# Kernel tuning notes

Hardware: AMD Instinct MI355X
Metric: run time of the kernel (lower is better)

The kernel has to match this reference:

```python
import jax, jax.numpy as jnp
import numpy as np

# MoE config (matches init_kwargs)
E = 32      # num_experts
K = 4       # num_experts_per_tok (top_k)
H = 1024    # hidden_size
I = 512     # moe_intermediate_size (shared expert uses I * num_shared_experts = I)
B, S = 2, 2048
T = B * S
C = 1024
ROUTED_SCALE = 1.0


def _silu_and_mul(gu):
    g, u = jnp.split(gu, 2, axis=-1)
    return jax.nn.silu(g) * u


def setup_inputs() -> dict:
    key = jax.random.key(0)
    ks = jax.random.split(key, 6)
    s = 0.02
    return {
        "hidden_states": jax.random.normal(ks[0], (B, S, H), jnp.float32),
        "gate_w": jax.random.normal(ks[1], (E, H), jnp.float32) * s,
        "w_gate_up": jax.random.normal(ks[2], (E, H, 2 * I), jnp.float32) * s,
        "w_down": jax.random.normal(ks[3], (E, I, H), jnp.float32) * s,
        "shared_w_gate_up": jax.random.normal(ks[4], (H, 2 * I), jnp.float32) * s,
        "shared_w_down": jax.random.normal(ks[5], (I, H), jnp.float32) * s,
    }


def reference(hidden_states, gate_w, w_gate_up, w_down, shared_w_gate_up, shared_w_down):
    b, s, h = hidden_states.shape
    x = hidden_states.reshape(-1, h)                      # [T, H]
    t = x.shape[0]

    # --- router: gate linear -> softmax -> top-k -> renormalize ---
    logits = x @ gate_w.T                                 # [T, E]
    probs = jax.nn.softmax(logits, axis=-1)
    topk_w, topk_idx = jax.lax.top_k(probs, K)            # [T, K]
    topk_w = topk_w / jnp.sum(topk_w, axis=-1, keepdims=True)  # norm_topk_prob
    topk_w = topk_w * ROUTED_SCALE

    # --- dispatch: sort (token, slot) assignments by expert, scatter into capacity buffer ---
    e_flat = topk_idx.reshape(-1)                         # [T*K]
    w_flat = topk_w.reshape(-1)
    t_flat = jnp.repeat(jnp.arange(t), K)
    order = jnp.argsort(e_flat)                           # stable sort by expert id
    e_s, w_s, t_s = e_flat[order], w_flat[order], t_flat[order]
    counts = jax.ops.segment_sum(jnp.ones_like(e_s), e_s, num_segments=E)
    starts = jnp.cumsum(counts) - counts                  # exclusive prefix sum
    pos = jnp.arange(t * K) - starts[e_s]                 # position within expert group
    slot = jnp.minimum(pos, C)                            # overflow -> trash slot C
    buf = jnp.zeros((E, C + 1, h), x.dtype).at[e_s, slot].set(x[t_s])

    # --- grouped expert MLP (silu-gated) ---
    gu = jnp.einsum('ech,ehi->eci', buf[:, :C], w_gate_up)        # [E, C, 2I]
    expert_out = jnp.einsum('eci,eih->ech', _silu_and_mul(gu), w_down)  # [E, C, H]
    expert_out = jnp.pad(expert_out, ((0, 0), (0, 1), (0, 0)))    # trash slot reads zero

    # --- combine: gather back, weight, scatter-add per token ---
    gate = jnp.where(pos < C, w_s, 0.0)[:, None]
    routed = jnp.zeros_like(x).at[t_s].add(expert_out[e_s, slot] * gate)

    # --- shared expert MLP ---
    shared = _silu_and_mul(x @ shared_w_gate_up) @ shared_w_down

    return (routed + shared).reshape(b, s, h)
```

## Files before the change

### kernel.cpp

```cpp
#include <hip/hip_runtime.h>
#include <cstdint>
#include <cstddef>

#define NEXP   32
#define TOPK   4
#define HD     1024
#define ID     512
#define TT     4096
#define CAP    1024
#define SHARED_BASE (NEXP*CAP)
#define NSLOT  (NEXP*CAP + TT)
#define MAXTILES 320

#define KSPLIT 16
#define KCH    64
#define KSUB   32

typedef __attribute__((ext_vector_type(4))) float f32x4;
typedef __bf16 bf16x8 __attribute__((ext_vector_type(8)));

__device__ __forceinline__ unsigned short f2bf(float f) {
    union { float f; unsigned int u; } v; v.f = f;
    unsigned int u = v.u;
    u = (u + 0x7FFFu + ((u >> 16) & 1u)) >> 16;
    return (unsigned short)u;
}
__device__ __forceinline__ float bf2f(unsigned short s) {
    union { unsigned int u; float f; } v; v.u = ((unsigned int)s) << 16;
    return v.f;
}

#define GLOAD_LDS16(g, l)                                                     \
    __builtin_amdgcn_global_load_lds(                                         \
        (__attribute__((address_space(1))) void*)(g),                         \
        (__attribute__((address_space(3))) void*)(l), 16, 0, 0)

__global__ void k_transpose_bf16(const float* __restrict__ src,
                                 const float* __restrict__ srcS,
                                 unsigned short* __restrict__ dst,
                                 int K, int N) {
    __shared__ float ld[64][65];
    const size_t esz = (size_t)K * N;
    const int z = blockIdx.z;
    const float* s = (z < NEXP) ? src + (size_t)z * esz : srcS;
    dst += (size_t)z * esz;
    const int n0 = blockIdx.x * 64, k0 = blockIdx.y * 64;
    const int tid = threadIdx.x;
    const int c4 = (tid & 15) * 4;
    const int rbase = tid >> 4;
#pragma unroll
    for (int p = 0; p < 4; p++) {
        int row = rbase + p * 16;
        float4 v = *(const float4*)(s + (size_t)(k0 + row) * N + n0 + c4);
        ld[row][c4 + 0] = v.x; ld[row][c4 + 1] = v.y;
        ld[row][c4 + 2] = v.z; ld[row][c4 + 3] = v.w;
    }
    __syncthreads();
    const int n  = tid >> 2;
    const int ks = (tid & 3) * 16;
    unsigned short tmp[16];
#pragma unroll
    for (int i = 0; i < 16; i++) tmp[i] = f2bf(ld[ks + i][n]);
    uint4 a, b;
    a.x = tmp[0] | (tmp[1] << 16);  a.y = tmp[2] | (tmp[3] << 16);
    a.z = tmp[4] | (tmp[5] << 16);  a.w = tmp[6] | (tmp[7] << 16);
    b.x = tmp[8] | (tmp[9] << 16);  b.y = tmp[10] | (tmp[11] << 16);
    b.z = tmp[12] | (tmp[13] << 16); b.w = tmp[14] | (tmp[15] << 16);
    unsigned short* op = dst + (size_t)(n0 + n) * K + k0 + ks;
    *(uint4*)op = a;
    *(uint4*)(op + 8) = b;
}

__global__ __launch_bounds__(256)
void k_logits(const float* __restrict__ x, const float* __restrict__ gw,
              float* __restrict__ part, unsigned short* __restrict__ xb) {
    __shared__ float xsT[KSUB][260];
    __shared__ float gsT[KSUB][36];
    const int tid = threadIdx.x;
    const int lane = tid & 63, wv = tid >> 6;
    const int tg = lane >> 2, eg = lane & 3;
    const int t0 = blockIdx.x * 256;
    const int kbase = blockIdx.y * KCH;
    const int tbase = wv * 64 + tg * 4;
    const int ebase = eg * 8;

    float acc[4][8];
#pragma unroll
    for (int j = 0; j < 4; j++)
#pragma unroll
        for (int i = 0; i < 8; i++) acc[j][i] = 0.f;

    for (int ks = 0; ks < KCH; ks += KSUB) {
        const int k0 = kbase + ks;
        if (ks > 0) __syncthreads();
#pragma unroll
        for (int p = 0; p < 8; p++) {
            int vid = p * 256 + tid;
            int t = vid >> 3, kq = (vid & 7) * 4;
            float4 v = *(const float4*)(x + (size_t)(t0 + t) * HD + k0 + kq);
            xsT[kq + 0][t] = v.x; xsT[kq + 1][t] = v.y;
            xsT[kq + 2][t] = v.z; xsT[kq + 3][t] = v.w;
            ushort4 o;
            o.x = f2bf(v.x); o.y = f2bf(v.y); o.z = f2bf(v.z); o.w = f2bf(v.w);
            *(ushort4*)(xb + (size_t)(t0 + t) * HD + k0 + kq) = o;
        }
#pragma unroll
        for (int p = 0; p < 4; p++) {
            int vid = p * 256 + tid;
            int e = vid >> 5, k = vid & 31;
            gsT[k][e] = gw[(size_t)e * HD + k0 + k];
        }
        __syncthreads();
#pragma unroll 4
        for (int k = 0; k < KSUB; k++) {
            float4 xv = *(const float4*)&xsT[k][tbase];
            float4 g0 = *(const float4*)&gsT[k][ebase];
            float4 g1 = *(const float4*)&gsT[k][ebase + 4];
            float xa[4] = {xv.x, xv.y, xv.z, xv.w};
#pragma unroll
            for (int j = 0; j < 4; j++) {
                acc[j][0] += xa[j] * g0.x; acc[j][1] += xa[j] * g0.y;
                acc[j][2] += xa[j] * g0.z; acc[j][3] += xa[j] * g0.w;
                acc[j][4] += xa[j] * g1.x; acc[j][5] += xa[j] * g1.y;
                acc[j][6] += xa[j] * g1.z; acc[j][7] += xa[j] * g1.w;
            }
        }
    }
    const size_t base = ((size_t)blockIdx.y * TT + (t0 + tbase)) * 32 + ebase;
#pragma unroll
    for (int j = 0; j < 4; j++) {
        float4 w0, w1;
        w0.x = acc[j][0]; w0.y = acc[j][1]; w0.z = acc[j][2]; w0.w = acc[j][3];
        w1.x = acc[j][4]; w1.y = acc[j][5]; w1.z = acc[j][6]; w1.w = acc[j][7];
        *(float4*)(part + base + (size_t)j * 32) = w0;
        *(float4*)(part + base + (size_t)j * 32 + 4) = w1;
    }
}

__global__ __launch_bounds__(256)
void k_topk(const float* __restrict__ part,
            int* __restrict__ choice, float* __restrict__ cw,
            int* __restrict__ tok, float* __restrict__ wgt) {
    const int lane = threadIdx.x & 63, wv = threadIdx.x >> 6;
    const int t = blockIdx.x * 4 + wv;
    const int e = lane & 31;
    const int sbase = (lane >> 5) * 8;
    float v = 0.f;
#pragma unroll
    for (int s = 0; s < 8; s++)
        v += part[((size_t)(sbase + s) * TT + t) * 32 + e];
    v += __shfl_xor(v, 32);
    float sc = (lane < 32) ? v : -INFINITY;

    float lv[TOPK]; int le[TOPK];
#pragma unroll
    for (int r = 0; r < TOPK; r++) {
        float m = sc;
#pragma unroll
        for (int d = 1; d < 64; d <<= 1) m = fmaxf(m, __shfl_xor(m, d));
        unsigned long long ball = __ballot(sc == m);
        int widx = __ffsll(ball) - 1;
        lv[r] = m; le[r] = widx;
        if (lane == widx) sc = -INFINITY;
    }
    if (lane == 0) {
        float wv4[TOPK], wsum = 0.f;
#pragma unroll
        for (int r = 0; r < TOPK; r++) { wv4[r] = __expf(lv[r] - lv[0]); wsum += wv4[r]; }
#pragma unroll
        for (int r = 0; r < TOPK; r++) {
            choice[t * TOPK + r] = le[r];
            cw[t * TOPK + r] = wv4[r] / wsum;
        }
        tok[SHARED_BASE + t] = t;
        wgt[SHARED_BASE + t] = 1.0f;
    }
}

__global__ __launch_bounds__(1024)
void k_assign(const int* __restrict__ choice, const float* __restrict__ cw,
              int* __restrict__ cnt, int* __restrict__ tok,
              float* __restrict__ wgt, int* __restrict__ smap) {
    const int e = blockIdx.x;
    const int tid = threadIdx.x, lane = tid & 63, wv = tid >> 6;
    __shared__ int wtot[16];
    int running = 0;
    for (int it = 0; it < (TT * TOPK) / 1024; it++) {
        const int i = it * 1024 + tid;
        const bool match = (choice[i] == e);
        unsigned long long ball = __ballot(match);
        int wt = __popcll(ball);
        int wpre = __popcll(ball & ((1ull << lane) - 1ull));
        if (lane == 0) wtot[wv] = wt;
        __syncthreads();
        int woff = 0, tot = 0;
#pragma unroll
        for (int w = 0; w < 16; w++) { int c = wtot[w]; tot += c; if (w < wv) woff += c; }
        int pos = running + woff + wpre;
        running += tot;
        __syncthreads();
        if (match) {
            if (pos < CAP) {
                int slot = e * CAP + pos;
                tok[slot] = i >> 2;
                wgt[slot] = cw[i];
                smap[i] = slot;
            } else {
                smap[i] = -1;
            }
        }
    }
    if (tid == 0) cnt[e] = min(running, CAP);
}

template <int KD, bool GATHER, bool SILU>
__global__ __launch_bounds__(256)
void k_moe_gemm(const unsigned short* __restrict__ Ab,
                const unsigned short* __restrict__ Bt,
                unsigned short* __restrict__ Cout,
                const int* __restrict__ tok,
                const int* __restrict__ cnt) {
    const int tid  = threadIdx.x;
    const int lane = tid & 63;
    const int wv   = tid >> 6;

    int c_l = (lane < NEXP) ? min(cnt[lane], CAP) : ((lane == NEXP) ? TT : 0);
    int nt_l = (c_l + 127) >> 7;
    int pre = nt_l;
#pragma unroll
    for (int d = 1; d < 64; d <<= 1) {
        int up = __shfl_up(pre, d);
        if (lane >= d) pre += up;
    }
    const int ntl = __shfl(pre, 63);
    const int chunk = (ntl + 7) >> 3;
    const int c_xcd = blockIdx.x;
    const int qy = blockIdx.y;
    if ((qy >> 3) >= chunk) return;
    const int j = c_xcd * chunk + (qy >> 3);
    if (j >= ntl) return;
    const int nt = qy & 7;
    const int start_l = pre - nt_l;
    const bool mine = (j >= start_l) && (j < start_l + nt_l);
    const unsigned long long bl = __ballot(mine);
    const int e_lane = __ffsll((long long)bl) - 1;
    const int e  = e_lane;
    const int mt = j - __shfl(start_l, e_lane);
    const int cE = __shfl(c_l, e_lane);

    const int slotbase = (e < NEXP) ? e * CAP : SHARED_BASE;
    const int m0 = mt * 128;
    const int rowsv = min(128, cE - m0);

    const unsigned short* Bte = Bt + (size_t)e * (1024 * KD);

    __shared__ unsigned short As[3][128 * 32];
    __shared__ unsigned short Bs[3][128 * 32];

    const int rr  = lane >> 2;
    const int seg = (lane & 3) ^ ((lane >> 3) & 3);
    const int r0 = wv * 32 + rr;
    const int r1 = r0 + 16;

    int ga0 = m0 + r0, ga1 = m0 + r1;
    int ra0, ra1;
    if (GATHER) {
        ra0 = (ga0 < cE) ? tok[slotbase + ga0] : 0;
        ra1 = (ga1 < cE) ? tok[slotbase + ga1] : 0;
    } else {
        ra0 = slotbase + ga0;
        ra1 = slotbase + ga1;
    }
    const unsigned short* ap0 = Ab + (size_t)ra0 * KD + seg * 8;
    const unsigned short* ap1 = Ab + (size_t)ra1 * KD + seg * 8;

    int br0, br1;
    if (SILU) {
        int in0 = r0 & 63, in1 = r1 & 63;
        int c0 = nt * 64 + (r0 >> 6) * 32 + (in0 & 31);
        int c1 = nt * 64 + (r1 >> 6) * 32 + (in1 & 31);
        br0 = (in0 < 32) ? c0 : 512 + c0;
        br1 = (in1 < 32) ? c1 : 512 + c1;
    } else {
        br0 = nt * 128 + r0;
        br1 = nt * 128 + r1;
    }
    const unsigned short* bp0 = Bte + (size_t)br0 * KD + seg * 8;
    const unsigned short* bp1 = Bte + (size_t)br1 * KD + seg * 8;

    const int aoff0 = (wv * 32) * 32, aoff1 = (wv * 32 + 16) * 32;

    f32x4 acc[4][4];
#pragma unroll
    for (int i = 0; i < 4; i++)
#pragma unroll
        for (int j2 = 0; j2 < 4; j2++) acc[i][j2] = (f32x4)(0.0f);

    const int mrow = lane & 15;
    const int quad = lane >> 4;
    const int wm = wv >> 1, wn = wv & 1;
    const int sw = (quad ^ ((mrow >> 1) & 3)) * 8;

    const int aRdOff = (wm * 64 + mrow) * 32 + sw;
    const int bRdOff = (wn * 64 + mrow) * 32 + sw;

    GLOAD_LDS16(ap0, As[0] + aoff0);
    GLOAD_LDS16(ap1, As[0] + aoff1);
    GLOAD_LDS16(bp0, Bs[0] + aoff0);
    GLOAD_LDS16(bp1, Bs[0] + aoff1);
    GLOAD_LDS16(ap0 + 32, As[1] + aoff0);
    GLOAD_LDS16(ap1 + 32, As[1] + aoff1);
    GLOAD_LDS16(bp0 + 32, Bs[1] + aoff0);
    GLOAD_LDS16(bp1 + 32, Bs[1] + aoff1);

    int p = 0;
    for (int k0 = 0; k0 < KD; k0 += 32) {
        if (k0 + 32 < KD) {
            asm volatile("s_waitcnt vmcnt(4) lgkmcnt(0)" ::: "memory");
        } else {
            asm volatile("s_waitcnt vmcnt(0) lgkmcnt(0)" ::: "memory");
        }
        __builtin_amdgcn_s_barrier();
        asm volatile("" ::: "memory");

        const int kn = k0 + 64;
        if (kn < KD) {
            int pw = p + 2; if (pw >= 3) pw -= 3;
            GLOAD_LDS16(ap0 + kn, As[pw] + aoff0);
            GLOAD_LDS16(ap1 + kn, As[pw] + aoff1);
            GLOAD_LDS16(bp0 + kn, Bs[pw] + aoff0);
            GLOAD_LDS16(bp1 + kn, Bs[pw] + aoff1);
        }

        bf16x8 af[4], bf[4];
#pragma unroll
        for (int i = 0; i < 4; i++) {
            af[i] = *(const bf16x8*)(As[p] + aRdOff + i * 16 * 32);
            bf[i] = *(const bf16x8*)(Bs[p] + bRdOff + i * 16 * 32);
        }
#pragma unroll
        for (int mi = 0; mi < 4; mi++)
#pragma unroll
            for (int nj = 0; nj < 4; nj++)
                acc[mi][nj] = __builtin_amdgcn_mfma_f32_16x16x32_bf16(
                    af[mi], bf[nj], acc[mi][nj], 0, 0, 0);
        p++; if (p >= 3) p = 0;
    }

    if (SILU) {
#pragma unroll
        for (int mi = 0; mi < 4; mi++)
#pragma unroll
            for (int nj = 0; nj < 2; nj++) {
                f32x4 g = acc[mi][nj];
                f32x4 u = acc[mi][nj + 2];
#pragma unroll
                for (int r = 0; r < 4; r++) {
                    int rloc = wm * 64 + mi * 16 + quad * 4 + r;
                    if (rloc < rowsv) {
                        float gv = g[r], uv = u[r];
                        float a = (gv / (1.f + __expf(-gv))) * uv;
                        int c = nt * 64 + wn * 32 + nj * 16 + mrow;
                        Cout[(size_t)(slotbase + m0 + rloc) * ID + c] = f2bf(a);
                    }
                }
            }
    } else {
#pragma unroll
        for (int mi = 0; mi < 4; mi++)
#pragma unroll
            for (int nj = 0; nj < 4; nj++) {
                f32x4 v = acc[mi][nj];
#pragma unroll
                for (int r = 0; r < 4; r++) {
                    int rloc = wm * 64 + mi * 16 + quad * 4 + r;
                    if (rloc < rowsv) {
                        int c = nt * 128 + wn * 64 + nj * 16 + mrow;
                        Cout[(size_t)(slotbase + m0 + rloc) * HD + c] = f2bf(v[r]);
                    }
                }
            }
    }
}

__global__ __launch_bounds__(256)
void k_combine(const unsigned short* __restrict__ eout,
               const int* __restrict__ smap,
               const float* __restrict__ wgt,
               float* __restrict__ out) {
    const int t = blockIdx.x;
    const int h0 = threadIdx.x * 4;
    ushort4 q = *(const ushort4*)(eout + (size_t)(SHARED_BASE + t) * HD + h0);
    float a0 = bf2f(q.x), a1 = bf2f(q.y), a2 = bf2f(q.z), a3 = bf2f(q.w);
#pragma unroll
    for (int r = 0; r < TOPK; r++) {
        int slot = smap[t * TOPK + r];
        if (slot >= 0) {
            float w = wgt[slot];
            ushort4 e4 = *(const ushort4*)(eout + (size_t)slot * HD + h0);
            a0 += w * bf2f(e4.x); a1 += w * bf2f(e4.y);
            a2 += w * bf2f(e4.z); a3 += w * bf2f(e4.w);
        }
    }
    float4 o; o.x = a0; o.y = a1; o.z = a2; o.w = a3;
    *(float4*)(out + (size_t)t * HD + h0) = o;
}

extern "C" void kernel_launch(void* const* d_in, const int* in_sizes, int n_in,
                              void* d_out, int out_size, void* d_ws, size_t ws_size,
                              hipStream_t stream) {
    const float* x   = (const float*)d_in[0];
    const float* gw  = (const float*)d_in[1];
    const float* wgu = (const float*)d_in[2];
    const float* wdn = (const float*)d_in[3];
    const float* sgu = (const float*)d_in[4];
    const float* sdn = (const float*)d_in[5];
    float* out = (float*)d_out;

    char* w = (char*)d_ws;
    size_t off = 0;
    int* cnt = (int*)(w + off);                       off += 256;
    unsigned short* xb     = (unsigned short*)(w + off); off += (size_t)TT * HD * 2;
    unsigned short* wgup_t = (unsigned short*)(w + off); off += (size_t)33 * 1024 * 1024 * 2;
    unsigned short* wdn_t  = (unsigned short*)(w + off); off += (size_t)33 * 1024 * 512 * 2;
    unsigned short* act    = (unsigned short*)(w + off); off += (size_t)NSLOT * ID * 2;
    unsigned short* eout   = (unsigned short*)(w + off); off += (size_t)NSLOT * HD * 2;
    int*   tok    = (int*)(w + off);   off += (size_t)NSLOT * 4;
    float* wgt    = (float*)(w + off); off += (size_t)NSLOT * 4;
    int*   smap   = (int*)(w + off);   off += (size_t)TT * TOPK * 4;
    int*   choice = (int*)(w + off);   off += (size_t)TT * TOPK * 4;
    float* cw     = (float*)(w + off); off += (size_t)TT * TOPK * 4;

    float* part = (float*)eout;

    k_transpose_bf16<<<dim3(16, 16, 33), 256, 0, stream>>>(wgu, sgu, wgup_t, 1024, 1024);
    k_transpose_bf16<<<dim3(16, 8, 33),  256, 0, stream>>>(wdn, sdn, wdn_t, 512, 1024);

    k_logits<<<dim3(16, KSPLIT), 256, 0, stream>>>(x, gw, part, xb);
    k_topk<<<TT / 4, 256, 0, stream>>>(part, choice, cw, tok, wgt);
    k_assign<<<NEXP, 1024, 0, stream>>>(choice, cw, cnt, tok, wgt, smap);

    k_moe_gemm<1024, true, true><<<dim3(8, MAXTILES), 256, 0, stream>>>(xb, wgup_t, act, tok, cnt);
    k_moe_gemm<512, false, false><<<dim3(8, MAXTILES), 256, 0, stream>>>(act, wdn_t, eout, tok, cnt);

    k_combine<<<TT, 256, 0, stream>>>(eout, smap, wgt, out);
}
```

Before: 430.9 us.

## Enlarge MoE GEMM tiles to 256x256 with 8 waves and 4-stage pipeline

The grouped expert GEMMs now use 256x256 output tiles computed by 512-thread blocks (8 waves, each covering 128x64), instead of 128x128 tiles with 4 waves. The K loop becomes a 4-buffer LDS pipeline with split A/B prefetch, interleaved half-tile MFMA phases, s_setprio and explicit barriers. The aim is more data reuse per tile and better overlap of loads with MFMA work. In exchange it uses more LDS (128KB) and registers, allowing only one block per CU, and partial tiles on experts with few tokens waste more work with fewer total tiles.

```diff
diff --git a/kernel.cpp b/kernel.cpp
--- a/kernel.cpp
+++ b/kernel.cpp
@@ -10,7 +10,7 @@
 #define CAP    1024
 #define SHARED_BASE (NEXP*CAP)
 #define NSLOT  (NEXP*CAP + TT)
-#define MAXTILES 320
+#define GRIDY  80
 
 #define KSPLIT 16
 #define KCH    64
@@ -213,8 +213,59 @@
     if (tid == 0) cnt[e] = min(running, CAP);
 }
 
+#define GEMM_ITER(T, PF, W)                                                    \
+{                                                                              \
+    const unsigned short* Ar = &As[(T) & 3][0];                                \
+    const unsigned short* Br = &Bs[(T) & 3][0];                                \
+    const int kn = ((T) + 3) * 32;                                             \
+    bf16x8 af[8], bf[4];                                                       \
+    _Pragma("unroll")                                                          \
+    for (int i = 0; i < 4; i++) {                                              \
+        af[i] = *(const bf16x8*)(Ar + aRdOff + i * 512);                       \
+        bf[i] = *(const bf16x8*)(Br + bRdOff + i * 512);                       \
+    }                                                                          \
+    if (PF) {                                                                  \
+        GLOAD_LDS16(ap0 + kn, &As[((T) + 3) & 3][0] + aoff0);                  \
+        GLOAD_LDS16(ap1 + kn, &As[((T) + 3) & 3][0] + aoff1);                  \
+    }                                                                          \
+    __builtin_amdgcn_s_barrier();                                              \
+    asm volatile("s_waitcnt lgkmcnt(0)" ::: "memory");                         \
+    __builtin_amdgcn_sched_barrier(0);                                         \
+    __builtin_amdgcn_s_setprio(1);                                             \
+    _Pragma("unroll")                                                          \
+    for (int mi = 0; mi < 4; mi++)                                             \
+        _Pragma("unroll")                                                      \
+        for (int nj = 0; nj < 4; nj++)                                         \
+            acc[mi][nj] = __builtin_amdgcn_mfma_f32_16x16x32_bf16(             \
+                af[mi], bf[nj], acc[mi][nj], 0, 0, 0);                         \
+    __builtin_amdgcn_s_setprio(0);                                             \
+    __builtin_amdgcn_s_barrier();                                              \
+    _Pragma("unroll")                                                          \
+    for (int i = 4; i < 8; i++)                                                \
+        af[i] = *(const bf16x8*)(Ar + aRdOff + i * 512);                       \
+    if (PF) {                                                                  \
+        GLOAD_LDS16(bp0 + kn, &Bs[((T) + 3) & 3][0] + aoff0);                  \
+        GLOAD_LDS16(bp1 + kn, &Bs[((T) + 3) & 3][0] + aoff1);                  \
+    }                                                                          \
+    __builtin_amdgcn_s_barrier();                                              \
+    asm volatile("s_waitcnt lgkmcnt(0)" ::: "memory");                         \
+    __builtin_amdgcn_sched_barrier(0);                                         \
+    __builtin_amdgcn_s_setprio(1);                                             \
+    _Pragma("unroll")                                                          \
+    for (int mi = 4; mi < 8; mi++)                                             \
+        _Pragma("unroll")                                                      \
+        for (int nj = 0; nj < 4; nj++)                                         \
+            acc[mi][nj] = __builtin_amdgcn_mfma_f32_16x16x32_bf16(             \
+                af[mi], bf[nj], acc[mi][nj], 0, 0, 0);                         \
+    __builtin_amdgcn_s_setprio(0);                                             \
+    if ((W) == 8)      asm volatile("s_waitcnt vmcnt(8)" ::: "memory");        \
+    else if ((W) == 4) asm volatile("s_waitcnt vmcnt(4)" ::: "memory");        \
+    else if ((W) == 0) asm volatile("s_waitcnt vmcnt(0)" ::: "memory");        \
+    if ((W) >= 0) __builtin_amdgcn_s_barrier();                                \
+}
+
 template <int KD, bool GATHER, bool SILU>
-__global__ __launch_bounds__(256)
+__global__ __launch_bounds__(512, 1)
 void k_moe_gemm(const unsigned short* __restrict__ Ab,
                 const unsigned short* __restrict__ Bt,
                 unsigned short* __restrict__ Cout,
@@ -225,7 +276,7 @@
     const int wv   = tid >> 6;
 
     int c_l = (lane < NEXP) ? min(cnt[lane], CAP) : ((lane == NEXP) ? TT : 0);
-    int nt_l = (c_l + 127) >> 7;
+    int nt_l = (c_l + 255) >> 8;
     int pre = nt_l;
 #pragma unroll
     for (int d = 1; d < 64; d <<= 1) {
@@ -236,10 +287,10 @@
     const int chunk = (ntl + 7) >> 3;
     const int c_xcd = blockIdx.x;
     const int qy = blockIdx.y;
-    if ((qy >> 3) >= chunk) return;
-    const int j = c_xcd * chunk + (qy >> 3);
+    if ((qy >> 2) >= chunk) return;
+    const int j = c_xcd * chunk + (qy >> 2);
     if (j >= ntl) return;
-    const int nt = qy & 7;
+    const int nt = qy & 3;
     const int start_l = pre - nt_l;
     const bool mine = (j >= start_l) && (j < start_l + nt_l);
     const unsigned long long bl = __ballot(mine);
@@ -249,13 +300,13 @@
     const int cE = __shfl(c_l, e_lane);
 
     const int slotbase = (e < NEXP) ? e * CAP : SHARED_BASE;
-    const int m0 = mt * 128;
-    const int rowsv = min(128, cE - m0);
+    const int m0 = mt * 256;
+    const int rowsv = min(256, cE - m0);
 
     const unsigned short* Bte = Bt + (size_t)e * (1024 * KD);
 
-    __shared__ unsigned short As[3][128 * 32];
-    __shared__ unsigned short Bs[3][128 * 32];
+    __shared__ unsigned short As[4][256 * 32];
+    __shared__ unsigned short Bs[4][256 * 32];
 
     const int rr  = lane >> 2;
     const int seg = (lane & 3) ^ ((lane >> 3) & 3);
@@ -277,105 +328,78 @@
     int br0, br1;
     if (SILU) {
         int in0 = r0 & 63, in1 = r1 & 63;
-        int c0 = nt * 64 + (r0 >> 6) * 32 + (in0 & 31);
-        int c1 = nt * 64 + (r1 >> 6) * 32 + (in1 & 31);
+        int c0 = nt * 128 + (r0 >> 6) * 32 + (in0 & 31);
+        int c1 = nt * 128 + (r1 >> 6) * 32 + (in1 & 31);
         br0 = (in0 < 32) ? c0 : 512 + c0;
         br1 = (in1 < 32) ? c1 : 512 + c1;
     } else {
-        br0 = nt * 128 + r0;
-        br1 = nt * 128 + r1;
+        br0 = nt * 256 + r0;
+        br1 = nt * 256 + r1;
     }
     const unsigned short* bp0 = Bte + (size_t)br0 * KD + seg * 8;
     const unsigned short* bp1 = Bte + (size_t)br1 * KD + seg * 8;
 
     const int aoff0 = (wv * 32) * 32, aoff1 = (wv * 32 + 16) * 32;
 
-    f32x4 acc[4][4];
-#pragma unroll
-    for (int i = 0; i < 4; i++)
+    f32x4 acc[8][4];
+#pragma unroll
+    for (int i = 0; i < 8; i++)
 #pragma unroll
         for (int j2 = 0; j2 < 4; j2++) acc[i][j2] = (f32x4)(0.0f);
 
     const int mrow = lane & 15;
     const int quad = lane >> 4;
-    const int wm = wv >> 1, wn = wv & 1;
+    const int wm = wv >> 2, wn = wv & 3;
     const int sw = (quad ^ ((mrow >> 1) & 3)) * 8;
 
-    const int aRdOff = (wm * 64 + mrow) * 32 + sw;
+    const int aRdOff = (wm * 128 + mrow) * 32 + sw;
     const int bRdOff = (wn * 64 + mrow) * 32 + sw;
 
-    GLOAD_LDS16(ap0, As[0] + aoff0);
-    GLOAD_LDS16(ap1, As[0] + aoff1);
-    GLOAD_LDS16(bp0, Bs[0] + aoff0);
-    GLOAD_LDS16(bp1, Bs[0] + aoff1);
-    GLOAD_LDS16(ap0 + 32, As[1] + aoff0);
-    GLOAD_LDS16(ap1 + 32, As[1] + aoff1);
-    GLOAD_LDS16(bp0 + 32, Bs[1] + aoff0);
-    GLOAD_LDS16(bp1 + 32, Bs[1] + aoff1);
-
-    int p = 0;
-    for (int k0 = 0; k0 < KD; k0 += 32) {
-        if (k0 + 32 < KD) {
-            asm volatile("s_waitcnt vmcnt(4) lgkmcnt(0)" ::: "memory");
-        } else {
-            asm volatile("s_waitcnt vmcnt(0) lgkmcnt(0)" ::: "memory");
-        }
-        __builtin_amdgcn_s_barrier();
-        asm volatile("" ::: "memory");
-
-        const int kn = k0 + 64;
-        if (kn < KD) {
-            int pw = p + 2; if (pw >= 3) pw -= 3;
-            GLOAD_LDS16(ap0 + kn, As[pw] + aoff0);
-            GLOAD_LDS16(ap1 + kn, As[pw] + aoff1);
-            GLOAD_LDS16(bp0 + kn, Bs[pw] + aoff0);
-            GLOAD_LDS16(bp1 + kn, Bs[pw] + aoff1);
-        }
-
-        bf16x8 af[4], bf[4];
-#pragma unroll
-        for (int i = 0; i < 4; i++) {
-            af[i] = *(const bf16x8*)(As[p] + aRdOff + i * 16 * 32);
-            bf[i] = *(const bf16x8*)(Bs[p] + bRdOff + i * 16 * 32);
-        }
-#pragma unroll
-        for (int mi = 0; mi < 4; mi++)
-#pragma unroll
-            for (int nj = 0; nj < 4; nj++)
-                acc[mi][nj] = __builtin_amdgcn_mfma_f32_16x16x32_bf16(
-                    af[mi], bf[nj], acc[mi][nj], 0, 0, 0);
-        p++; if (p >= 3) p = 0;
-    }
+#pragma unroll
+    for (int c = 0; c < 3; c++) {
+        GLOAD_LDS16(ap0 + c * 32, &As[c][0] + aoff0);
+        GLOAD_LDS16(ap1 + c * 32, &As[c][0] + aoff1);
+        GLOAD_LDS16(bp0 + c * 32, &Bs[c][0] + aoff0);
+        GLOAD_LDS16(bp1 + c * 32, &Bs[c][0] + aoff1);
+    }
+    asm volatile("s_waitcnt vmcnt(8)" ::: "memory");
+    __builtin_amdgcn_s_barrier();
+
+    const int NTCH = KD / 32;
+    for (int t = 0; t < NTCH - 3; ++t) GEMM_ITER(t, true, 8);
+    GEMM_ITER(NTCH - 3, false, 4);
+    GEMM_ITER(NTCH - 2, false, 0);
+    GEMM_ITER(NTCH - 1, false, -1);
 
     if (SILU) {
 #pragma unroll
-        for (int mi = 0; mi < 4; mi++)
+        for (int mi = 0; mi < 8; mi++)
 #pragma unroll
             for (int nj = 0; nj < 2; nj++) {
                 f32x4 g = acc[mi][nj];
                 f32x4 u = acc[mi][nj + 2];
 #pragma unroll
                 for (int r = 0; r < 4; r++) {
-                    int rloc = wm * 64 + mi * 16 + quad * 4 + r;
+                    int rloc = wm * 128 + mi * 16 + quad * 4 + r;
                     if (rloc < rowsv) {
                         float gv = g[r], uv = u[r];
                         float a = (gv / (1.f + __expf(-gv))) * uv;
-                        int c = nt * 64 + wn * 32 + nj * 16 + mrow;
+                        int c = nt * 128 + wn * 32 + nj * 16 + mrow;
                         Cout[(size_t)(slotbase + m0 + rloc) * ID + c] = f2bf(a);
                     }
                 }
             }
     } else {
 #pragma unroll
-        for (int mi = 0; mi < 4; mi++)
+        for (int mi = 0; mi < 8; mi++)
 #pragma unroll
             for (int nj = 0; nj < 4; nj++) {
                 f32x4 v = acc[mi][nj];
 #pragma unroll
                 for (int r = 0; r < 4; r++) {
-                    int rloc = wm * 64 + mi * 16 + quad * 4 + r;
+                    int rloc = wm * 128 + mi * 16 + quad * 4 + r;
                     if (rloc < rowsv) {
-                        int c = nt * 128 + wn * 64 + nj * 16 + mrow;
+                        int c = nt * 256 + wn * 64 + nj * 16 + mrow;
                         Cout[(size_t)(slotbase + m0 + rloc) * HD + c] = f2bf(v[r]);
                     }
                 }
@@ -440,8 +464,8 @@
     k_topk<<<TT / 4, 256, 0, stream>>>(part, choice, cw, tok, wgt);
     k_assign<<<NEXP, 1024, 0, stream>>>(choice, cw, cnt, tok, wgt, smap);
 
-    k_moe_gemm<1024, true, true><<<dim3(8, MAXTILES), 256, 0, stream>>>(xb, wgup_t, act, tok, cnt);
-    k_moe_gemm<512, false, false><<<dim3(8, MAXTILES), 256, 0, stream>>>(act, wdn_t, eout, tok, cnt);
+    k_moe_gemm<1024, true, true><<<dim3(8, GRIDY), 512, 0, stream>>>(xb, wgup_t, act, tok, cnt);
+    k_moe_gemm<512, false, false><<<dim3(8, GRIDY), 512, 0, stream>>>(act, wdn_t, eout, tok, cnt);
 
     k_combine<<<TT, 256, 0, stream>>>(eout, smap, wgt, out);
 }
```

New measurement: 462.5 us. 1.07x slower.

## Switch grouped GEMM to 64-wide K tiles with double-buffered LDS

Applied to the files above, without the earlier changes.

The grouped expert GEMM kernel now stages K in chunks of 64 instead of 32, using two LDS buffers rather than a three-deep ring. Each chunk is loaded with four 16-byte global-to-LDS loads per thread per operand, under a new XOR swizzle over 8 segments. The wider chunk halves the number of barriers and waitcnt points per K sweep and runs two MFMA sub-steps per barrier. The trade-off is a shallower prefetch: each iteration waits for all outstanding loads (vmcnt(0)), so less global latency is hidden, and LDS use grows from 48KB to 64KB, which may lower occupancy.

```diff
diff --git a/kernel.cpp b/kernel.cpp
--- a/kernel.cpp
+++ b/kernel.cpp
@@ -254,41 +254,44 @@
 
     const unsigned short* Bte = Bt + (size_t)e * (1024 * KD);
 
-    __shared__ unsigned short As[3][128 * 32];
-    __shared__ unsigned short Bs[3][128 * 32];
-
-    const int rr  = lane >> 2;
-    const int seg = (lane & 3) ^ ((lane >> 3) & 3);
-    const int r0 = wv * 32 + rr;
-    const int r1 = r0 + 16;
-
-    int ga0 = m0 + r0, ga1 = m0 + r1;
-    int ra0, ra1;
-    if (GATHER) {
-        ra0 = (ga0 < cE) ? tok[slotbase + ga0] : 0;
-        ra1 = (ga1 < cE) ? tok[slotbase + ga1] : 0;
-    } else {
-        ra0 = slotbase + ga0;
-        ra1 = slotbase + ga1;
-    }
-    const unsigned short* ap0 = Ab + (size_t)ra0 * KD + seg * 8;
-    const unsigned short* ap1 = Ab + (size_t)ra1 * KD + seg * 8;
-
-    int br0, br1;
-    if (SILU) {
-        int in0 = r0 & 63, in1 = r1 & 63;
-        int c0 = nt * 64 + (r0 >> 6) * 32 + (in0 & 31);
-        int c1 = nt * 64 + (r1 >> 6) * 32 + (in1 & 31);
-        br0 = (in0 < 32) ? c0 : 512 + c0;
-        br1 = (in1 < 32) ? c1 : 512 + c1;
-    } else {
-        br0 = nt * 128 + r0;
-        br1 = nt * 128 + r1;
-    }
-    const unsigned short* bp0 = Bte + (size_t)br0 * KD + seg * 8;
-    const unsigned short* bp1 = Bte + (size_t)br1 * KD + seg * 8;
-
-    const int aoff0 = (wv * 32) * 32, aoff1 = (wv * 32 + 16) * 32;
+    __shared__ unsigned short As[2][128 * 64];
+    __shared__ unsigned short Bs[2][128 * 64];
+
+    const int rr8  = lane >> 3;
+    const int seg8 = (lane & 7) ^ rr8;
+
+    const unsigned short* ap[4];
+    const unsigned short* bp[4];
+#pragma unroll
+    for (int pp = 0; pp < 4; pp++) {
+        int r = wv * 32 + pp * 8 + rr8;
+        int ga = m0 + r;
+        int ra;
+        if (GATHER) {
+            ra = (ga < cE) ? tok[slotbase + ga] : 0;
+        } else {
+            ra = slotbase + ga;
+        }
+        ap[pp] = Ab + (size_t)ra * KD + seg8 * 8;
+        int br;
+        if (SILU) {
+            int in = r & 63;
+            int c = nt * 64 + (r >> 6) * 32 + (in & 31);
+            br = (in < 32) ? c : 512 + c;
+        } else {
+            br = nt * 128 + r;
+        }
+        bp[pp] = Bte + (size_t)br * KD + seg8 * 8;
+    }
+
+#define STAGE(P, K0)                                                          \
+    {                                                                         \
+        _Pragma("unroll")                                                     \
+        for (int pp = 0; pp < 4; pp++) {                                      \
+            GLOAD_LDS16(ap[pp] + (K0), &As[P][0] + (wv * 32 + pp * 8) * 64);  \
+            GLOAD_LDS16(bp[pp] + (K0), &Bs[P][0] + (wv * 32 + pp * 8) * 64);  \
+        }                                                                     \
+    }
 
     f32x4 acc[4][4];
 #pragma unroll
@@ -299,52 +302,40 @@
     const int mrow = lane & 15;
     const int quad = lane >> 4;
     const int wm = wv >> 1, wn = wv & 1;
-    const int sw = (quad ^ ((mrow >> 1) & 3)) * 8;
-
-    const int aRdOff = (wm * 64 + mrow) * 32 + sw;
-    const int bRdOff = (wn * 64 + mrow) * 32 + sw;
-
-    GLOAD_LDS16(ap0, As[0] + aoff0);
-    GLOAD_LDS16(ap1, As[0] + aoff1);
-    GLOAD_LDS16(bp0, Bs[0] + aoff0);
-    GLOAD_LDS16(bp1, Bs[0] + aoff1);
-    GLOAD_LDS16(ap0 + 32, As[1] + aoff0);
-    GLOAD_LDS16(ap1 + 32, As[1] + aoff1);
-    GLOAD_LDS16(bp0 + 32, Bs[1] + aoff0);
-    GLOAD_LDS16(bp1 + 32, Bs[1] + aoff1);
+    const int sw0 = ((quad ^ (mrow & 7)) * 8);
+
+    const int aRdBase = (wm * 64 + mrow) * 64;
+    const int bRdBase = (wn * 64 + mrow) * 64;
+
+    STAGE(0, 0);
 
     int p = 0;
-    for (int k0 = 0; k0 < KD; k0 += 32) {
-        if (k0 + 32 < KD) {
-            asm volatile("s_waitcnt vmcnt(4) lgkmcnt(0)" ::: "memory");
-        } else {
-            asm volatile("s_waitcnt vmcnt(0) lgkmcnt(0)" ::: "memory");
-        }
+    for (int k0 = 0; k0 < KD; k0 += 64) {
+        asm volatile("s_waitcnt vmcnt(0) lgkmcnt(0)" ::: "memory");
         __builtin_amdgcn_s_barrier();
         asm volatile("" ::: "memory");
 
-        const int kn = k0 + 64;
-        if (kn < KD) {
-            int pw = p + 2; if (pw >= 3) pw -= 3;
-            GLOAD_LDS16(ap0 + kn, As[pw] + aoff0);
-            GLOAD_LDS16(ap1 + kn, As[pw] + aoff1);
-            GLOAD_LDS16(bp0 + kn, Bs[pw] + aoff0);
-            GLOAD_LDS16(bp1 + kn, Bs[pw] + aoff1);
-        }
-
-        bf16x8 af[4], bf[4];
-#pragma unroll
-        for (int i = 0; i < 4; i++) {
-            af[i] = *(const bf16x8*)(As[p] + aRdOff + i * 16 * 32);
-            bf[i] = *(const bf16x8*)(Bs[p] + bRdOff + i * 16 * 32);
-        }
-#pragma unroll
-        for (int mi = 0; mi < 4; mi++)
-#pragma unroll
-            for (int nj = 0; nj < 4; nj++)
-                acc[mi][nj] = __builtin_amdgcn_mfma_f32_16x16x32_bf16(
-                    af[mi], bf[nj], acc[mi][nj], 0, 0, 0);
-        p++; if (p >= 3) p = 0;
+        if (k0 + 64 < KD) {
+            if (p == 0) STAGE(1, k0 + 64) else STAGE(0, k0 + 64);
+        }
+
+#pragma unroll
+        for (int kk = 0; kk < 2; kk++) {
+            const int swk = sw0 ^ (kk << 5);
+            bf16x8 af[4], bf[4];
+#pragma unroll
+            for (int i = 0; i < 4; i++) {
+                af[i] = *(const bf16x8*)(&As[p][0] + aRdBase + i * 16 * 64 + swk);
+                bf[i] = *(const bf16x8*)(&Bs[p][0] + bRdBase + i * 16 * 64 + swk);
+            }
+#pragma unroll
+            for (int mi = 0; mi < 4; mi++)
+#pragma unroll
+                for (int nj = 0; nj < 4; nj++)
+                    acc[mi][nj] = __builtin_amdgcn_mfma_f32_16x16x32_bf16(
+                        af[mi], bf[nj], acc[mi][nj], 0, 0, 0);
+        }
+        p ^= 1;
     }
 
     if (SILU) {
@@ -381,6 +372,7 @@
                 }
             }
     }
+#undef STAGE
 }
 
 __global__ __launch_bounds__(256)
```

Result: slower. 441.2 us (+2.4%).
